# Optimization experiments

Hardware: AMD Instinct MI355X
Metric: run time of the kernel (lower is better)

The kernel has to match this reference:

```python
import jax, jax.numpy as jnp
import numpy as np

MAX_GAP = 32  # n_index = 2*MAX_GAP+1 = 65


def setup_inputs() -> dict:
    key = jax.random.key(0)
    kW, kb = jax.random.split(key)
    B, S, E, N = 1, 1024, 128, 2 * MAX_GAP + 1
    idxs = jnp.arange(B * S, dtype=jnp.int64 if jax.config.jax_enable_x64 else jnp.int32).reshape(B, S)
    W = jax.random.normal(kW, (E, N), dtype=jnp.float32)  # nn.Linear weight (out, in)
    b = jax.random.normal(kb, (E,), dtype=jnp.float32)    # nn.Linear bias
    return {"idxs": idxs, "W": W, "b": b}


def reference(idxs, W, b):
    # pos_2d[b,i,j] = clip(idxs[b,j] - idxs[b,i], -max_gap, max_gap) + max_gap  in [0, n_index)
    pos = jnp.clip(idxs[:, None, :] - idxs[:, :, None], -MAX_GAP, MAX_GAP) + MAX_GAP  # (B,S,S)
    # onehot(pos) @ W.T + b  ==  row-gather from W.T plus bias (same math, no dense one-hot)
    return jnp.take(W.T, pos, axis=0) + b  # (B,S,S,E)
```

## Files before the change

### kernel.cpp

```cpp
#include <hip/hip_runtime.h>


#define MAXGAP 32
#define NIDX   65
#define EDIM   128
#define E4     32
#define PADE   132

typedef float f32x4 __attribute__((ext_vector_type(4)));

__global__ __launch_bounds__(256) void relpos2d_kernel(
    const int* __restrict__ idxs,
    const float* __restrict__ W,
    const float* __restrict__ bias,
    f32x4* __restrict__ out,
    int S)
{
    __shared__ float table[NIDX * PADE];
    __shared__ int   jidx[1024];

    for (int t = threadIdx.x; t < NIDX * EDIM; t += 256) {
        float w = W[t];
        int e = t / NIDX;
        int p = t - e * NIDX;
        table[p * PADE + e] = w + bias[e];
    }

    const int i = blockIdx.x;

    for (int t = threadIdx.x; t < S; t += 256)
        jidx[t] = idxs[t];

    __syncthreads();

    const int lane4 = threadIdx.x & 31;
    const int jsub  = threadIdx.x >> 5;
    const int idx_i = idxs[i];

    f32x4* __restrict__ orow = out + (size_t)i * S * E4;

    #pragma unroll 4
    for (int jj = 0; jj < S; jj += 8) {
        int j = jj + jsub;
        int d = jidx[j] - idx_i;
        d = d < -MAXGAP ? -MAXGAP : (d > MAXGAP ? MAXGAP : d);
        int p = d + MAXGAP;

        f32x4 v = reinterpret_cast<const f32x4*>(&table[p * PADE])[lane4];
        orow[(size_t)j * E4 + lane4] = v;
    }
}

extern "C" void kernel_launch(void* const* d_in, const int* in_sizes, int n_in,
                              void* d_out, int out_size, void* d_ws, size_t ws_size,
                              hipStream_t stream) {
    const int*   idxs = (const int*)  d_in[0];
    const float* W    = (const float*)d_in[1];
    const float* bias = (const float*)d_in[2];

    f32x4* out = (f32x4*)d_out;

    const int S    = in_sizes[0];
    const int grid = S;

    relpos2d_kernel<<<grid, 256, 0, stream>>>(idxs, W, bias, out, S);
}
```

Measured before the change: 105.0 us.

## Flatten output rows into a grid-stride loop over a fixed grid

```diff
diff --git a/kernel.cpp b/kernel.cpp
--- a/kernel.cpp
+++ b/kernel.cpp
@@ -6,6 +6,7 @@
 #define EDIM   128
 #define E4     32
 #define PADE   132
+#define WPB    4
 
 typedef float f32x4 __attribute__((ext_vector_type(4)));
 
@@ -14,10 +15,10 @@
     const float* __restrict__ W,
     const float* __restrict__ bias,
     f32x4* __restrict__ out,
-    int S)
+    int S, int logS, int totalRows)
 {
     __shared__ float table[NIDX * PADE];
-    __shared__ int   jidx[1024];
+    __shared__ int   sidx[1024];
 
     for (int t = threadIdx.x; t < NIDX * EDIM; t += 256) {
         float w = W[t];
@@ -26,28 +27,29 @@
         table[p * PADE + e] = w + bias[e];
     }
 
-    const int i = blockIdx.x;
-
     for (int t = threadIdx.x; t < S; t += 256)
-        jidx[t] = idxs[t];
+        sidx[t] = idxs[t];
 
     __syncthreads();
 
-    const int lane4 = threadIdx.x & 31;
-    const int jsub  = threadIdx.x >> 5;
-    const int idx_i = idxs[i];
-
-    f32x4* __restrict__ orow = out + (size_t)i * S * E4;
+    const int lane  = threadIdx.x & 63;
+    const int lane4 = lane & 31;
+    const int half  = lane >> 5;
+    const int wid   = blockIdx.x * WPB + (threadIdx.x >> 6);
+    const int rowsPerStep = gridDim.x * WPB * 2;
 
     #pragma unroll 4
-    for (int jj = 0; jj < S; jj += 8) {
-        int j = jj + jsub;
-        int d = jidx[j] - idx_i;
+    for (int r0 = wid * 2; r0 < totalRows; r0 += rowsPerStep) {
+        int r = r0 + half;
+        int i = r >> logS;
+        int j = r & (S - 1);
+
+        int d = sidx[j] - sidx[i];
         d = d < -MAXGAP ? -MAXGAP : (d > MAXGAP ? MAXGAP : d);
         int p = d + MAXGAP;
 
         f32x4 v = reinterpret_cast<const f32x4*>(&table[p * PADE])[lane4];
-        orow[(size_t)j * E4 + lane4] = v;
+        out[(size_t)r * E4 + lane4] = v;
     }
 }
 
@@ -60,8 +62,11 @@
 
     f32x4* out = (f32x4*)d_out;
 
-    const int S    = in_sizes[0];
-    const int grid = S;
+    const int S         = in_sizes[0];
+    int logS = 0; while ((1 << logS) < S) ++logS;
+    const int totalRows = S * S;
+    const int grid      = 2048;
 
-    relpos2d_kernel<<<grid, 256, 0, stream>>>(idxs, W, bias, out, S);
+    relpos2d_kernel<<<grid, 256, 0, stream>>>(
+        idxs, W, bias, out, S, logS, totalRows);
 }
```

Measured after the change: 127.0 us. +20.9%, slower.
